# Optimization experiments

Measured on AMD Instinct MI355X. Metric: run time of the kernel, lower is better.

## Reference

```python
import jax, jax.numpy as jnp
import numpy as np

N_NODES = 20000
N_EDGES = 640000
NODE_DIM = 128
EDGE_DIM = 64
HID = 128  # must equal NODE_DIM (index_add_ into zeros_like(node_feat) in the original)
EPS = 1e-8


def setup_inputs() -> dict:
    key = jax.random.key(0)
    ks = jax.random.split(key, 16)
    s = 0.05
    return {
        "node_feat": jax.random.normal(ks[0], (N_NODES, NODE_DIM), jnp.float32),
        "edge_index": jax.random.randint(ks[1], (2, N_EDGES), 0, N_NODES, jnp.int32),
        "edge_attr": jax.random.normal(ks[2], (N_EDGES, EDGE_DIM), jnp.float32),
        "coords": jax.random.normal(ks[3], (N_NODES, 3), jnp.float32),
        # edge_mlp: Linear(2*node+edge -> hid), SiLU, Linear(hid -> hid), SiLU
        "eW1": jax.random.normal(ks[4], (2 * NODE_DIM + EDGE_DIM, HID), jnp.float32) * s,
        "eb1": jnp.zeros((HID,), jnp.float32),
        "eW2": jax.random.normal(ks[5], (HID, HID), jnp.float32) * s,
        "eb2": jnp.zeros((HID,), jnp.float32),
        # node_mlp: Linear(node+hid -> hid), SiLU, Linear(hid -> node)
        "nW1": jax.random.normal(ks[6], (NODE_DIM + HID, HID), jnp.float32) * s,
        "nb1": jnp.zeros((HID,), jnp.float32),
        "nW2": jax.random.normal(ks[7], (HID, NODE_DIM), jnp.float32) * s,
        "nb2": jnp.zeros((NODE_DIM,), jnp.float32),
        # coord_mlp: Linear(hid -> hid//2), SiLU, Linear(hid//2 -> 1)
        "cW1": jax.random.normal(ks[8], (HID, HID // 2), jnp.float32) * s,
        "cb1": jnp.zeros((HID // 2,), jnp.float32),
        "cW2": jax.random.normal(ks[9], (HID // 2, 1), jnp.float32) * s,
        "cb2": jnp.zeros((1,), jnp.float32),
    }


def reference(node_feat, edge_index, edge_attr, coords,
              eW1, eb1, eW2, eb2, nW1, nb1, nW2, nb2, cW1, cb1, cW2, cb2):
    silu = jax.nn.silu
    src, dst = edge_index[0], edge_index[1]

    # edge messages: gather -> concat -> 2-layer MLP (SiLU after both layers)
    edge_feat = jnp.concatenate([node_feat[src], node_feat[dst], edge_attr], axis=-1)  # [E, 2*node+edge]
    edge_message = silu(silu(edge_feat @ eW1 + eb1) @ eW2 + eb2)  # [E, hid]

    # aggregate messages per destination node (index_add_)
    aggr_message = jax.ops.segment_sum(edge_message, dst, num_segments=N_NODES)  # [N, hid]

    # node update (residual)
    node_input = jnp.concatenate([node_feat, aggr_message], axis=-1)
    node_update = silu(node_input @ nW1 + nb1) @ nW2 + nb2
    updated_nodes = node_feat + node_update

    # coordinate update: per-edge scalar weight times unit direction, scattered to dst
    coord_weights = silu(edge_message @ cW1 + cb1) @ cW2 + cb2  # [E, 1]
    coord_diff = coords[src] - coords[dst]  # [E, 3]
    coord_diff = coord_diff / (jnp.linalg.norm(coord_diff, axis=-1, keepdims=True) + EPS)
    coord_update = jax.ops.segment_sum(coord_weights * coord_diff, dst, num_segments=N_NODES)
    updated_coords = coords + coord_update

    return updated_nodes, updated_coords
```

## Files before the change

kernel.cpp:

```cpp
#include <hip/hip_runtime.h>
#include <math.h>

#define N_NODES 20000
#define N_EDGES 640000
#define D 128
#define ED 64
#define EPS 1e-8f
#define MT 64
#define EMT 128

#define RSTRIDE 136
#define HSTRIDE 136
#define NSTRIDE 264

#define EW2_OFF 40960
#define CW1_OFF 57344
#define NW1_OFF 65536
#define NW2_OFF 98304
#define NFBF_OFF 114688
#define CSR_OFF  2674688

typedef __attribute__((ext_vector_type(8))) short bf16x8;
typedef __attribute__((ext_vector_type(4))) short bf16x4;
typedef __attribute__((ext_vector_type(16))) float f32x16;

__device__ __forceinline__ float silu_f(float x) {
    return __fdividef(x, 1.0f + __expf(-x));
}

__device__ __forceinline__ short f2bf(float f) {
    union { float f; unsigned u; } v; v.f = f;
    unsigned r = v.u + 0x7FFFu + ((v.u >> 16) & 1u);
    return (short)(r >> 16);
}
__device__ __forceinline__ float bf2f(short s) {
    union { unsigned u; float f; } v;
    v.u = ((unsigned)(unsigned short)s) << 16;
    return v.f;
}
__device__ __forceinline__ unsigned cvt_pk_bf16(float lo, float hi) {
    unsigned r;
    asm("v_cvt_pk_bf16_f32 %0, %1, %2" : "=v"(r) : "v"(lo), "v"(hi));
    return r;
}

__global__ __launch_bounds__(256)
void prep_kernel(const float* __restrict__ eW1, const float* __restrict__ eW2,
                 const float* __restrict__ cW1, const float* __restrict__ nW1,
                 const float* __restrict__ nW2,
                 const float* __restrict__ node_feat,
                 const float* __restrict__ coords,
                 short* __restrict__ wsf, short* __restrict__ nfbf,
                 int* __restrict__ cnt,
                 float* __restrict__ nodes_io, float* __restrict__ out_coords) {
    const int t = blockIdx.x * blockDim.x + threadIdx.x;
    const int nthr = gridDim.x * blockDim.x;

    if (t < 224 * 64) {
        int f = t >> 6, lane = t & 63;
        const float* src; int kc, nt, ncol; size_t dst;
        if (f < 80)       {              src = eW1; kc = f >> 2;  nt = f & 3;  ncol = 128; dst = (size_t)f * 512; }
        else if (f < 112) { int g=f-80;  src = eW2; kc = g >> 2;  nt = g & 3;  ncol = 128; dst = EW2_OFF + (size_t)g * 512; }
        else if (f < 128) { int g=f-112; src = cW1; kc = g >> 1;  nt = g & 1;  ncol = 64;  dst = CW1_OFF + (size_t)g * 512; }
        else if (f < 192) { int g=f-128; src = nW1; kc = g >> 2;  nt = g & 3;  ncol = 128; dst = NW1_OFF + (size_t)g * 512; }
        else              { int g=f-192; src = nW2; kc = g >> 2;  nt = g & 3;  ncol = 128; dst = NW2_OFF + (size_t)g * 512; }
        int col = nt * 32 + (lane & 31);
        int k0  = kc * 16 + (lane >> 5) * 8;
        bf16x8 o;
        #pragma unroll
        for (int j = 0; j < 8; ++j) o[j] = f2bf(src[(size_t)(k0 + j) * ncol + col]);
        *(bf16x8*)&wsf[dst + (size_t)lane * 8] = o;
    }
    for (int idx = t; idx < N_NODES * D / 8; idx += nthr) {
        const float* s = node_feat + (size_t)idx * 8;
        float4 f0 = *(const float4*)s, f1 = *(const float4*)(s + 4);
        bf16x8 pk;
        pk[0]=f2bf(f0.x); pk[1]=f2bf(f0.y); pk[2]=f2bf(f0.z); pk[3]=f2bf(f0.w);
        pk[4]=f2bf(f1.x); pk[5]=f2bf(f1.y); pk[6]=f2bf(f1.z); pk[7]=f2bf(f1.w);
        *(bf16x8*)&nfbf[(size_t)idx * 8] = pk;
    }
    for (int idx = t; idx < N_NODES * D / 4; idx += nthr) {
        float4 z; z.x = 0.f; z.y = 0.f; z.z = 0.f; z.w = 0.f;
        *(float4*)&nodes_io[(size_t)idx * 4] = z;
    }
    for (int idx = t; idx < N_NODES; idx += nthr) cnt[idx] = 0;
    for (int idx = t; idx < N_NODES * 3; idx += nthr)
        out_coords[idx] = coords[idx];
}

__global__ __launch_bounds__(256)
void hist_kernel(const int* __restrict__ edge_index, int* __restrict__ cnt) {
    int t = blockIdx.x * blockDim.x + threadIdx.x;
    if (t < N_EDGES) atomicAdd(&cnt[edge_index[N_EDGES + t]], 1);
}

#define SCAN_T 1024
#define SCAN_C 20
__global__ __launch_bounds__(SCAN_T)
void scan_kernel(const int* __restrict__ cnt, int* __restrict__ cursor) {
    __shared__ int lc[N_NODES];
    __shared__ int part[SCAN_T];
    const int t = threadIdx.x;
    for (int i = t * 4; i < N_NODES; i += SCAN_T * 4)
        *(int4*)&lc[i] = *(const int4*)&cnt[i];
    __syncthreads();
    const int base = t * SCAN_C;
    int s = 0;
    #pragma unroll
    for (int i = 0; i < SCAN_C; ++i) {
        int idx = base + i;
        if (idx < N_NODES) s += lc[idx];
    }
    part[t] = s;
    __syncthreads();
    for (int off = 1; off < SCAN_T; off <<= 1) {
        int v = (t >= off) ? part[t - off] : 0;
        __syncthreads();
        part[t] += v;
        __syncthreads();
    }
    int run = part[t] - s;
    #pragma unroll
    for (int i = 0; i < SCAN_C; ++i) {
        int idx = base + i;
        if (idx < N_NODES) { int c = lc[idx]; lc[idx] = run; run += c; }
    }
    __syncthreads();
    for (int i = t * 4; i < N_NODES; i += SCAN_T * 4)
        *(int4*)&cursor[i] = *(const int4*)&lc[i];
}

__global__ __launch_bounds__(256)
void scatter_kernel(const int* __restrict__ edge_index,
                    int* __restrict__ cursor, int* __restrict__ perm) {
    int t = blockIdx.x * blockDim.x + threadIdx.x;
    if (t < N_EDGES) {
        int d = edge_index[N_EDGES + t];
        int pos = atomicAdd(&cursor[d], 1);
        perm[pos] = t;
    }
}

__global__ __launch_bounds__(256, 4)
void edge_kernel(const short* __restrict__ nfbf,
                 const int* __restrict__ edge_index,
                 const int* __restrict__ perm,
                 const float* __restrict__ edge_attr,
                 const float* __restrict__ coords,
                 const float* __restrict__ eb1, const float* __restrict__ eb2,
                 const float* __restrict__ cb1, const float* __restrict__ cW2,
                 const float* __restrict__ cb2,
                 const short* __restrict__ wsf,
                 float* __restrict__ aggr_nodes, float* __restrict__ out_coords) {
    __shared__ __align__(16) short R[EMT * RSTRIDE];
    __shared__ int s_src[EMT], s_dst[EMT];
    __shared__ float s_wgt[EMT];
    __shared__ float s_cv[EMT][3];
    __shared__ char s_segend[EMT];
    __shared__ __align__(16) float s_eb1[D], s_eb2[D];
    __shared__ __align__(16) float s_cb1[ED], s_cw2[ED];

    const int tid = threadIdx.x;
    const int E0 = blockIdx.x * EMT;

    const int ie = tid >> 1, p = tid & 1;
    const int eid  = perm[E0 + ie];
    const int esrc = edge_index[eid];
    const int edst = edge_index[N_EDGES + eid];
    if (p == 0) { s_src[ie] = esrc; s_dst[ie] = edst; }
    if (tid < EMT) s_wgt[tid] = 0.0f;
    if (tid < 128) { s_eb1[tid] = eb1[tid]; s_eb2[tid] = eb2[tid]; }
    else if (tid < 192) { int i = tid - 128; s_cb1[i] = cb1[i]; s_cw2[i] = cW2[i]; }

    {
        const short* row = nfbf + (size_t)esrc * D + p * 64;
        short* dstp = &R[ie * RSTRIDE + p * 64];
        #pragma unroll
        for (int c = 0; c < 8; ++c)
            *(bf16x8*)&dstp[c * 8] = *(const bf16x8*)&row[c * 8];
    }
    __syncthreads();
    if (tid < EMT)
        s_segend[tid] = (tid == EMT - 1) || (s_dst[tid] != s_dst[tid + 1]);

    const int lane  = tid & 63;
    const int wv    = tid >> 6;
    const int n0q   = wv & 1;
    const int m0a   = (wv >> 1) * 64;
    const int m0b   = m0a + 32;
    const int l31   = lane & 31;
    const int khalf = lane >> 5;

    const bf16x8* W1 = (const bf16x8*)wsf;
    const bf16x8* W2 = (const bf16x8*)(wsf + EW2_OFF);
    const bf16x8* W3 = (const bf16x8*)(wsf + CW1_OFF);

    f32x16 acc00, acc01, acc10, acc11;
    #pragma unroll
    for (int r = 0; r < 16; ++r) { acc00[r]=0.f; acc01[r]=0.f; acc10[r]=0.f; acc11[r]=0.f; }

    #pragma unroll
    for (int kcl = 0; kcl < 8; ++kcl) {
        bf16x8 a0 = *(const bf16x8*)&R[(m0a + l31) * RSTRIDE + kcl * 16 + khalf * 8];
        bf16x8 a1 = *(const bf16x8*)&R[(m0b + l31) * RSTRIDE + kcl * 16 + khalf * 8];
        bf16x8 b0 = W1[((kcl) * 4 + n0q * 2 + 0) * 64 + lane];
        bf16x8 b1 = W1[((kcl) * 4 + n0q * 2 + 1) * 64 + lane];
        acc00 = __builtin_amdgcn_mfma_f32_32x32x16_bf16(b0, a0, acc00, 0, 0, 0);
        acc01 = __builtin_amdgcn_mfma_f32_32x32x16_bf16(b1, a0, acc01, 0, 0, 0);
        acc10 = __builtin_amdgcn_mfma_f32_32x32x16_bf16(b0, a1, acc10, 0, 0, 0);
        acc11 = __builtin_amdgcn_mfma_f32_32x32x16_bf16(b1, a1, acc11, 0, 0, 0);
    }
    __syncthreads();

    {
        const short* row = nfbf + (size_t)edst * D + p * 64;
        short* dstp = &R[ie * RSTRIDE + p * 64];
        #pragma unroll
        for (int c = 0; c < 8; ++c)
            *(bf16x8*)&dstp[c * 8] = *(const bf16x8*)&row[c * 8];
    }
    __syncthreads();

    #pragma unroll
    for (int kcl = 0; kcl < 8; ++kcl) {
        bf16x8 a0 = *(const bf16x8*)&R[(m0a + l31) * RSTRIDE + kcl * 16 + khalf * 8];
        bf16x8 a1 = *(const bf16x8*)&R[(m0b + l31) * RSTRIDE + kcl * 16 + khalf * 8];
        bf16x8 b0 = W1[((8 + kcl) * 4 + n0q * 2 + 0) * 64 + lane];
        bf16x8 b1 = W1[((8 + kcl) * 4 + n0q * 2 + 1) * 64 + lane];
        acc00 = __builtin_amdgcn_mfma_f32_32x32x16_bf16(b0, a0, acc00, 0, 0, 0);
        acc01 = __builtin_amdgcn_mfma_f32_32x32x16_bf16(b1, a0, acc01, 0, 0, 0);
        acc10 = __builtin_amdgcn_mfma_f32_32x32x16_bf16(b0, a1, acc10, 0, 0, 0);
        acc11 = __builtin_amdgcn_mfma_f32_32x32x16_bf16(b1, a1, acc11, 0, 0, 0);
    }
    __syncthreads();

    {
        const float* arow = edge_attr + (size_t)eid * ED + p * 32;
        #pragma unroll
        for (int c = 0; c < 2; ++c) {
            float4 a0 = *(const float4*)&arow[c * 16 + 0];
            float4 a1 = *(const float4*)&arow[c * 16 + 4];
            float4 a2 = *(const float4*)&arow[c * 16 + 8];
            float4 a3 = *(const float4*)&arow[c * 16 + 12];
            uint4 q;
            q.x = cvt_pk_bf16(a0.x, a0.y); q.y = cvt_pk_bf16(a0.z, a0.w);
            q.z = cvt_pk_bf16(a1.x, a1.y); q.w = cvt_pk_bf16(a1.z, a1.w);
            *(uint4*)&R[ie * RSTRIDE + p * 32 + c * 16] = q;
            q.x = cvt_pk_bf16(a2.x, a2.y); q.y = cvt_pk_bf16(a2.z, a2.w);
            q.z = cvt_pk_bf16(a3.x, a3.y); q.w = cvt_pk_bf16(a3.z, a3.w);
            *(uint4*)&R[ie * RSTRIDE + p * 32 + c * 16 + 8] = q;
        }
    }
    __syncthreads();

    #pragma unroll
    for (int kcl = 0; kcl < 4; ++kcl) {
        bf16x8 a0 = *(const bf16x8*)&R[(m0a + l31) * RSTRIDE + kcl * 16 + khalf * 8];
        bf16x8 a1 = *(const bf16x8*)&R[(m0b + l31) * RSTRIDE + kcl * 16 + khalf * 8];
        bf16x8 b0 = W1[((16 + kcl) * 4 + n0q * 2 + 0) * 64 + lane];
        bf16x8 b1 = W1[((16 + kcl) * 4 + n0q * 2 + 1) * 64 + lane];
        acc00 = __builtin_amdgcn_mfma_f32_32x32x16_bf16(b0, a0, acc00, 0, 0, 0);
        acc01 = __builtin_amdgcn_mfma_f32_32x32x16_bf16(b1, a0, acc01, 0, 0, 0);
        acc10 = __builtin_amdgcn_mfma_f32_32x32x16_bf16(b0, a1, acc10, 0, 0, 0);
        acc11 = __builtin_amdgcn_mfma_f32_32x32x16_bf16(b1, a1, acc11, 0, 0, 0);
    }
    __syncthreads();

    #pragma unroll
    for (int mt = 0; mt < 2; ++mt) {
        int erow = (mt ? m0b : m0a) + l31;
        #pragma unroll
        for (int nt = 0; nt < 2; ++nt) {
            f32x16 A = mt ? (nt ? acc11 : acc10) : (nt ? acc01 : acc00);
            int base = n0q * 64 + nt * 32 + 4 * khalf;
            #pragma unroll
            for (int g = 0; g < 4; ++g) {
                int n = base + 8 * g;
                float4 b4 = *(const float4*)&s_eb1[n];
                uint2 dd;
                dd.x = cvt_pk_bf16(silu_f(A[4*g+0] + b4.x), silu_f(A[4*g+1] + b4.y));
                dd.y = cvt_pk_bf16(silu_f(A[4*g+2] + b4.z), silu_f(A[4*g+3] + b4.w));
                *(uint2*)&R[erow * RSTRIDE + n] = dd;
            }
        }
    }
    __syncthreads();

    #pragma unroll
    for (int r = 0; r < 16; ++r) { acc00[r]=0.f; acc01[r]=0.f; acc10[r]=0.f; acc11[r]=0.f; }
    #pragma unroll
    for (int kc = 0; kc < 8; ++kc) {
        bf16x8 a0 = *(const bf16x8*)&R[(m0a + l31) * RSTRIDE + kc * 16 + khalf * 8];
        bf16x8 a1 = *(const bf16x8*)&R[(m0b + l31) * RSTRIDE + kc * 16 + khalf * 8];
        bf16x8 b0 = W2[(kc * 4 + n0q * 2 + 0) * 64 + lane];
        bf16x8 b1 = W2[(kc * 4 + n0q * 2 + 1) * 64 + lane];
        acc00 = __builtin_amdgcn_mfma_f32_32x32x16_bf16(b0, a0, acc00, 0, 0, 0);
        acc01 = __builtin_amdgcn_mfma_f32_32x32x16_bf16(b1, a0, acc01, 0, 0, 0);
        acc10 = __builtin_amdgcn_mfma_f32_32x32x16_bf16(b0, a1, acc10, 0, 0, 0);
        acc11 = __builtin_amdgcn_mfma_f32_32x32x16_bf16(b1, a1, acc11, 0, 0, 0);
    }
    __syncthreads();

    #pragma unroll
    for (int mt = 0; mt < 2; ++mt) {
        int erow = (mt ? m0b : m0a) + l31;
        #pragma unroll
        for (int nt = 0; nt < 2; ++nt) {
            f32x16 A = mt ? (nt ? acc11 : acc10) : (nt ? acc01 : acc00);
            int base = n0q * 64 + nt * 32 + 4 * khalf;
            #pragma unroll
            for (int g = 0; g < 4; ++g) {
                int n = base + 8 * g;
                float4 b4 = *(const float4*)&s_eb2[n];
                uint2 dd;
                dd.x = cvt_pk_bf16(silu_f(A[4*g+0] + b4.x), silu_f(A[4*g+1] + b4.y));
                dd.y = cvt_pk_bf16(silu_f(A[4*g+2] + b4.z), silu_f(A[4*g+3] + b4.w));
                *(uint2*)&R[erow * RSTRIDE + n] = dd;
            }
        }
    }
    __syncthreads();

    {
        f32x16 c0, c1;
        #pragma unroll
        for (int r = 0; r < 16; ++r) { c0[r] = 0.f; c1[r] = 0.f; }
        #pragma unroll
        for (int kc = 0; kc < 8; ++kc) {
            bf16x8 a0 = *(const bf16x8*)&R[(m0a + l31) * RSTRIDE + kc * 16 + khalf * 8];
            bf16x8 a1 = *(const bf16x8*)&R[(m0b + l31) * RSTRIDE + kc * 16 + khalf * 8];
            bf16x8 b  = W3[(kc * 2 + n0q) * 64 + lane];
            c0 = __builtin_amdgcn_mfma_f32_32x32x16_bf16(b, a0, c0, 0, 0, 0);
            c1 = __builtin_amdgcn_mfma_f32_32x32x16_bf16(b, a1, c1, 0, 0, 0);
        }
        float s0 = 0.f, s1 = 0.f;
        int nb = n0q * 32 + 4 * khalf;
        #pragma unroll
        for (int g = 0; g < 4; ++g) {
            float4 b4 = *(const float4*)&s_cb1[nb + 8 * g];
            float4 w4 = *(const float4*)&s_cw2[nb + 8 * g];
            s0 += silu_f(c0[4*g+0] + b4.x) * w4.x + silu_f(c0[4*g+1] + b4.y) * w4.y
                + silu_f(c0[4*g+2] + b4.z) * w4.z + silu_f(c0[4*g+3] + b4.w) * w4.w;
            s1 += silu_f(c1[4*g+0] + b4.x) * w4.x + silu_f(c1[4*g+1] + b4.y) * w4.y
                + silu_f(c1[4*g+2] + b4.z) * w4.z + silu_f(c1[4*g+3] + b4.w) * w4.w;
        }
        s0 += __shfl_xor(s0, 32);
        s1 += __shfl_xor(s1, 32);
        if (khalf == 0) {
            atomicAdd(&s_wgt[m0a + l31], s0);
            atomicAdd(&s_wgt[m0b + l31], s1);
        }
    }
    __syncthreads();

    if (tid < EMT) {
        int e = tid;
        float wgt = s_wgt[e] + cb2[0];
        int s = s_src[e], d = s_dst[e];
        float dx = coords[s * 3 + 0] - coords[d * 3 + 0];
        float dy = coords[s * 3 + 1] - coords[d * 3 + 1];
        float dz = coords[s * 3 + 2] - coords[d * 3 + 2];
        float inv = __fdividef(wgt, sqrtf(dx * dx + dy * dy + dz * dz) + EPS);
        s_cv[e][0] = dx * inv; s_cv[e][1] = dy * inv; s_cv[e][2] = dz * inv;
    }
    __syncthreads();

    {
        int q  = tid & 31;
        int st = tid >> 5;
        int cc = q * 4;
        float a0 = 0.f, a1 = 0.f, a2 = 0.f, a3 = 0.f;
        #pragma unroll
        for (int r = 0; r < 16; ++r) {
            int e = st * 16 + r;
            bf16x4 m = *(const bf16x4*)&R[e * RSTRIDE + cc];
            a0 += bf2f(m[0]); a1 += bf2f(m[1]); a2 += bf2f(m[2]); a3 += bf2f(m[3]);
            if (s_segend[e]) {
                float* ap = &aggr_nodes[(size_t)s_dst[e] * D + cc];
                unsafeAtomicAdd(ap + 0, a0); unsafeAtomicAdd(ap + 1, a1);
                unsafeAtomicAdd(ap + 2, a2); unsafeAtomicAdd(ap + 3, a3);
                a0 = a1 = a2 = a3 = 0.f;
            }
        }
        int elast = st * 16 + 15;
        if (!s_segend[elast]) {
            float* ap = &aggr_nodes[(size_t)s_dst[elast] * D + cc];
            unsafeAtomicAdd(ap + 0, a0); unsafeAtomicAdd(ap + 1, a1);
            unsafeAtomicAdd(ap + 2, a2); unsafeAtomicAdd(ap + 3, a3);
        }
    }

    if (tid < EMT) {
        int e = tid;
        bool head = (e == 0) || (s_dst[e] != s_dst[e - 1]);
        if (head) {
            float sx = 0.f, sy = 0.f, sz = 0.f;
            int j = e;
            do {
                sx += s_cv[j][0]; sy += s_cv[j][1]; sz += s_cv[j][2];
                ++j;
            } while (j < EMT && s_dst[j] == s_dst[e]);
            int d = s_dst[e];
            unsafeAtomicAdd(&out_coords[d * 3 + 0], sx);
            unsafeAtomicAdd(&out_coords[d * 3 + 1], sy);
            unsafeAtomicAdd(&out_coords[d * 3 + 2], sz);
        }
    }
}

__global__ __launch_bounds__(256, 4)
void node_kernel(const float* __restrict__ node_feat,
                 const short* __restrict__ nfbf,
                 float* nodes_io,
                 const float* __restrict__ nb1, const float* __restrict__ nb2,
                 const short* __restrict__ wsf) {
    __shared__ __align__(16) short lds[MT * NSTRIDE];
    __shared__ __align__(16) float s_nb1[D], s_nb2[D];
    const int tid = threadIdx.x;
    const int N0 = blockIdx.x * MT;

    if (tid < 128) { s_nb1[tid] = nb1[tid]; s_nb2[tid] = nb2[tid]; }
    {
        int i = tid >> 2, p = tid & 3;
        int nid = N0 + i; if (nid > N_NODES - 1) nid = N_NODES - 1;
        const short* frow = nfbf + (size_t)nid * D;
        short* drow = &lds[i * NSTRIDE];
        #pragma unroll
        for (int c = 0; c < 4; ++c)
            *(bf16x8*)&drow[c * 32 + p * 8] = *(const bf16x8*)&frow[c * 32 + p * 8];
        const float* arow = nodes_io + (size_t)nid * D + p * 32;
        #pragma unroll
        for (int c = 0; c < 4; ++c) {
            float4 f0 = *(const float4*)&arow[c * 8];
            float4 f1 = *(const float4*)&arow[c * 8 + 4];
            bf16x8 pk;
            pk[0]=f2bf(f0.x); pk[1]=f2bf(f0.y); pk[2]=f2bf(f0.z); pk[3]=f2bf(f0.w);
            pk[4]=f2bf(f1.x); pk[5]=f2bf(f1.y); pk[6]=f2bf(f1.z); pk[7]=f2bf(f1.w);
            *(bf16x8*)&drow[128 + p * 32 + c * 8] = pk;
        }
    }
    __syncthreads();

    const int lane  = tid & 63;
    const int wv    = tid >> 6;
    const int m0    = (wv >> 1) * 32;
    const int n0q   = wv & 1;
    const int l31   = lane & 31;
    const int khalf = lane >> 5;

    const bf16x8* W1 = (const bf16x8*)(wsf + NW1_OFF);
    const bf16x8* W2 = (const bf16x8*)(wsf + NW2_OFF);

    {
        f32x16 acc0, acc1;
        #pragma unroll
        for (int r = 0; r < 16; ++r) { acc0[r] = 0.f; acc1[r] = 0.f; }
        #pragma unroll
        for (int kc = 0; kc < 16; ++kc) {
            bf16x8 a  = *(const bf16x8*)&lds[(m0 + l31) * NSTRIDE + kc * 16 + khalf * 8];
            bf16x8 b0 = W1[(kc * 4 + n0q * 2 + 0) * 64 + lane];
            bf16x8 b1 = W1[(kc * 4 + n0q * 2 + 1) * 64 + lane];
            acc0 = __builtin_amdgcn_mfma_f32_32x32x16_bf16(b0, a, acc0, 0, 0, 0);
            acc1 = __builtin_amdgcn_mfma_f32_32x32x16_bf16(b1, a, acc1, 0, 0, 0);
        }
        __syncthreads();
        int nrow = m0 + l31;
        #pragma unroll
        for (int nt = 0; nt < 2; ++nt) {
            f32x16 A = nt ? acc1 : acc0;
            int base = n0q * 64 + nt * 32 + 4 * khalf;
            #pragma unroll
            for (int g = 0; g < 4; ++g) {
                int n = base + 8 * g;
                float4 b4 = *(const float4*)&s_nb1[n];
                uint2 dd;
                dd.x = cvt_pk_bf16(silu_f(A[4*g+0] + b4.x), silu_f(A[4*g+1] + b4.y));
                dd.y = cvt_pk_bf16(silu_f(A[4*g+2] + b4.z), silu_f(A[4*g+3] + b4.w));
                *(uint2*)&lds[nrow * HSTRIDE + n] = dd;
            }
        }
    }
    __syncthreads();

    {
        f32x16 acc0, acc1;
        #pragma unroll
        for (int r = 0; r < 16; ++r) { acc0[r] = 0.f; acc1[r] = 0.f; }
        #pragma unroll
        for (int kc = 0; kc < 8; ++kc) {
            bf16x8 a  = *(const bf16x8*)&lds[(m0 + l31) * HSTRIDE + kc * 16 + khalf * 8];
            bf16x8 b0 = W2[(kc * 4 + n0q * 2 + 0) * 64 + lane];
            bf16x8 b1 = W2[(kc * 4 + n0q * 2 + 1) * 64 + lane];
            acc0 = __builtin_amdgcn_mfma_f32_32x32x16_bf16(b0, a, acc0, 0, 0, 0);
            acc1 = __builtin_amdgcn_mfma_f32_32x32x16_bf16(b1, a, acc1, 0, 0, 0);
        }
        int nid = N0 + m0 + l31;
        if (nid < N_NODES) {
            #pragma unroll
            for (int nt = 0; nt < 2; ++nt) {
                f32x16 A = nt ? acc1 : acc0;
                int base = n0q * 64 + nt * 32 + 4 * khalf;
                #pragma unroll
                for (int g = 0; g < 4; ++g) {
                    int n = base + 8 * g;
                    float4 b4  = *(const float4*)&s_nb2[n];
                    float4 rsd = *(const float4*)&node_feat[(size_t)nid * D + n];
                    float4 o;
                    o.x = A[4*g+0] + b4.x + rsd.x;
                    o.y = A[4*g+1] + b4.y + rsd.y;
                    o.z = A[4*g+2] + b4.z + rsd.z;
                    o.w = A[4*g+3] + b4.w + rsd.w;
                    *(float4*)&nodes_io[(size_t)nid * D + n] = o;
                }
            }
        }
    }
}

extern "C" void kernel_launch(void* const* d_in, const int* in_sizes, int n_in,
                              void* d_out, int out_size, void* d_ws, size_t ws_size,
                              hipStream_t stream) {
    const float* node_feat  = (const float*)d_in[0];
    const int*   edge_index = (const int*)d_in[1];
    const float* edge_attr  = (const float*)d_in[2];
    const float* coords     = (const float*)d_in[3];
    const float* eW1 = (const float*)d_in[4];
    const float* eb1 = (const float*)d_in[5];
    const float* eW2 = (const float*)d_in[6];
    const float* eb2 = (const float*)d_in[7];
    const float* nW1 = (const float*)d_in[8];
    const float* nb1 = (const float*)d_in[9];
    const float* nW2 = (const float*)d_in[10];
    const float* nb2 = (const float*)d_in[11];
    const float* cW1 = (const float*)d_in[12];
    const float* cb1 = (const float*)d_in[13];
    const float* cW2 = (const float*)d_in[14];
    const float* cb2 = (const float*)d_in[15];

    float* nodes_io   = (float*)d_out;
    float* out_coords = nodes_io + (size_t)N_NODES * D;
    short* wsf    = (short*)d_ws;
    short* nfbf   = wsf + NFBF_OFF;
    int*   cnt    = (int*)(wsf + CSR_OFF);
    int*   cursor = cnt + N_NODES;
    int*   perm   = cursor + N_NODES;

    prep_kernel<<<256, 256, 0, stream>>>(
        eW1, eW2, cW1, nW1, nW2, node_feat, coords,
        wsf, nfbf, cnt, nodes_io, out_coords);
    hist_kernel<<<N_EDGES / 256, 256, 0, stream>>>(edge_index, cnt);
    scan_kernel<<<1, SCAN_T, 0, stream>>>(cnt, cursor);
    scatter_kernel<<<N_EDGES / 256, 256, 0, stream>>>(edge_index, cursor, perm);
    edge_kernel<<<N_EDGES / EMT, 256, 0, stream>>>(
        nfbf, edge_index, perm, edge_attr, coords,
        eb1, eb2, cb1, cW2, cb2, wsf, nodes_io, out_coords);
    node_kernel<<<(N_NODES + MT - 1) / MT, 256, 0, stream>>>(
        node_feat, nfbf, nodes_io, nb1, nb2, wsf);
}
```

Measured before the change: 526.7 us.

## Give each wave full output width and chain MLP layers in registers

Result: slower. 625.0 us (+18.7%).

```diff
diff --git a/kernel.cpp b/kernel.cpp
--- a/kernel.cpp
+++ b/kernel.cpp
@@ -141,7 +141,7 @@
     }
 }
 
-__global__ __launch_bounds__(256, 4)
+__global__ __launch_bounds__(256, 3)
 void edge_kernel(const short* __restrict__ nfbf,
                  const int* __restrict__ edge_index,
                  const int* __restrict__ perm,
@@ -168,7 +168,6 @@
     const int esrc = edge_index[eid];
     const int edst = edge_index[N_EDGES + eid];
     if (p == 0) { s_src[ie] = esrc; s_dst[ie] = edst; }
-    if (tid < EMT) s_wgt[tid] = 0.0f;
     if (tid < 128) { s_eb1[tid] = eb1[tid]; s_eb2[tid] = eb2[tid]; }
     else if (tid < 192) { int i = tid - 128; s_cb1[i] = cb1[i]; s_cw2[i] = cW2[i]; }
 
@@ -185,30 +184,29 @@
 
     const int lane  = tid & 63;
     const int wv    = tid >> 6;
-    const int n0q   = wv & 1;
-    const int m0a   = (wv >> 1) * 64;
-    const int m0b   = m0a + 32;
+    const int m0    = wv * 32;
     const int l31   = lane & 31;
     const int khalf = lane >> 5;
+    const int erow  = m0 + l31;
 
     const bf16x8* W1 = (const bf16x8*)wsf;
     const bf16x8* W2 = (const bf16x8*)(wsf + EW2_OFF);
     const bf16x8* W3 = (const bf16x8*)(wsf + CW1_OFF);
 
-    f32x16 acc00, acc01, acc10, acc11;
-    #pragma unroll
-    for (int r = 0; r < 16; ++r) { acc00[r]=0.f; acc01[r]=0.f; acc10[r]=0.f; acc11[r]=0.f; }
+    f32x16 acc[4];
+    #pragma unroll
+    for (int nt = 0; nt < 4; ++nt)
+        #pragma unroll
+        for (int r = 0; r < 16; ++r) acc[nt][r] = 0.f;
 
     #pragma unroll
     for (int kcl = 0; kcl < 8; ++kcl) {
-        bf16x8 a0 = *(const bf16x8*)&R[(m0a + l31) * RSTRIDE + kcl * 16 + khalf * 8];
-        bf16x8 a1 = *(const bf16x8*)&R[(m0b + l31) * RSTRIDE + kcl * 16 + khalf * 8];
-        bf16x8 b0 = W1[((kcl) * 4 + n0q * 2 + 0) * 64 + lane];
-        bf16x8 b1 = W1[((kcl) * 4 + n0q * 2 + 1) * 64 + lane];
-        acc00 = __builtin_amdgcn_mfma_f32_32x32x16_bf16(b0, a0, acc00, 0, 0, 0);
-        acc01 = __builtin_amdgcn_mfma_f32_32x32x16_bf16(b1, a0, acc01, 0, 0, 0);
-        acc10 = __builtin_amdgcn_mfma_f32_32x32x16_bf16(b0, a1, acc10, 0, 0, 0);
-        acc11 = __builtin_amdgcn_mfma_f32_32x32x16_bf16(b1, a1, acc11, 0, 0, 0);
+        bf16x8 a = *(const bf16x8*)&R[erow * RSTRIDE + kcl * 16 + khalf * 8];
+        #pragma unroll
+        for (int nt = 0; nt < 4; ++nt) {
+            bf16x8 b = W1[(kcl * 4 + nt) * 64 + lane];
+            acc[nt] = __builtin_amdgcn_mfma_f32_32x32x16_bf16(b, a, acc[nt], 0, 0, 0);
+        }
     }
     __syncthreads();
 
@@ -223,14 +221,12 @@
 
     #pragma unroll
     for (int kcl = 0; kcl < 8; ++kcl) {
-        bf16x8 a0 = *(const bf16x8*)&R[(m0a + l31) * RSTRIDE + kcl * 16 + khalf * 8];
-        bf16x8 a1 = *(const bf16x8*)&R[(m0b + l31) * RSTRIDE + kcl * 16 + khalf * 8];
-        bf16x8 b0 = W1[((8 + kcl) * 4 + n0q * 2 + 0) * 64 + lane];
-        bf16x8 b1 = W1[((8 + kcl) * 4 + n0q * 2 + 1) * 64 + lane];
-        acc00 = __builtin_amdgcn_mfma_f32_32x32x16_bf16(b0, a0, acc00, 0, 0, 0);
-        acc01 = __builtin_amdgcn_mfma_f32_32x32x16_bf16(b1, a0, acc01, 0, 0, 0);
-        acc10 = __builtin_amdgcn_mfma_f32_32x32x16_bf16(b0, a1, acc10, 0, 0, 0);
-        acc11 = __builtin_amdgcn_mfma_f32_32x32x16_bf16(b1, a1, acc11, 0, 0, 0);
+        bf16x8 a = *(const bf16x8*)&R[erow * RSTRIDE + kcl * 16 + khalf * 8];
+        #pragma unroll
+        for (int nt = 0; nt < 4; ++nt) {
+            bf16x8 b = W1[((8 + kcl) * 4 + nt) * 64 + lane];
+            acc[nt] = __builtin_amdgcn_mfma_f32_32x32x16_bf16(b, a, acc[nt], 0, 0, 0);
+        }
     }
     __syncthreads();
 
@@ -255,101 +251,109 @@
 
     #pragma unroll
     for (int kcl = 0; kcl < 4; ++kcl) {
-        bf16x8 a0 = *(const bf16x8*)&R[(m0a + l31) * RSTRIDE + kcl * 16 + khalf * 8];
-        bf16x8 a1 = *(const bf16x8*)&R[(m0b + l31) * RSTRIDE + kcl * 16 + khalf * 8];
-        bf16x8 b0 = W1[((16 + kcl) * 4 + n0q * 2 + 0) * 64 + lane];
-        bf16x8 b1 = W1[((16 + kcl) * 4 + n0q * 2 + 1) * 64 + lane];
-        acc00 = __builtin_amdgcn_mfma_f32_32x32x16_bf16(b0, a0, acc00, 0, 0, 0);
-        acc01 = __builtin_amdgcn_mfma_f32_32x32x16_bf16(b1, a0, acc01, 0, 0, 0);
-        acc10 = __builtin_amdgcn_mfma_f32_32x32x16_bf16(b0, a1, acc10, 0, 0, 0);
-        acc11 = __builtin_amdgcn_mfma_f32_32x32x16_bf16(b1, a1, acc11, 0, 0, 0);
-    }
-    __syncthreads();
-
-    #pragma unroll
-    for (int mt = 0; mt < 2; ++mt) {
-        int erow = (mt ? m0b : m0a) + l31;
-        #pragma unroll
-        for (int nt = 0; nt < 2; ++nt) {
-            f32x16 A = mt ? (nt ? acc11 : acc10) : (nt ? acc01 : acc00);
-            int base = n0q * 64 + nt * 32 + 4 * khalf;
+        bf16x8 a = *(const bf16x8*)&R[erow * RSTRIDE + kcl * 16 + khalf * 8];
+        #pragma unroll
+        for (int nt = 0; nt < 4; ++nt) {
+            bf16x8 b = W1[((16 + kcl) * 4 + nt) * 64 + lane];
+            acc[nt] = __builtin_amdgcn_mfma_f32_32x32x16_bf16(b, a, acc[nt], 0, 0, 0);
+        }
+    }
+
+    uint2 pk[4][4];
+    #pragma unroll
+    for (int nt = 0; nt < 4; ++nt) {
+        #pragma unroll
+        for (int g = 0; g < 4; ++g) {
+            int n = nt * 32 + 4 * khalf + 8 * g;
+            float4 b4 = *(const float4*)&s_eb1[n];
+            pk[nt][g].x = cvt_pk_bf16(silu_f(acc[nt][4*g+0] + b4.x), silu_f(acc[nt][4*g+1] + b4.y));
+            pk[nt][g].y = cvt_pk_bf16(silu_f(acc[nt][4*g+2] + b4.z), silu_f(acc[nt][4*g+3] + b4.w));
+        }
+    }
+
+    {
+        f32x16 a2[4];
+        #pragma unroll
+        for (int nt = 0; nt < 4; ++nt)
+            #pragma unroll
+            for (int r = 0; r < 16; ++r) a2[nt][r] = 0.f;
+        #pragma unroll
+        for (int kc = 0; kc < 8; ++kc) {
+            const int nt = kc >> 1;
+            const int gE = (kc & 1) * 2;
+            const int gO = gE + 1;
+            uint2 own  = khalf ? pk[nt][gO] : pk[nt][gE];
+            uint2 send = khalf ? pk[nt][gE] : pk[nt][gO];
+            uint2 recv;
+            recv.x = (unsigned)__shfl_xor((int)send.x, 32);
+            recv.y = (unsigned)__shfl_xor((int)send.y, 32);
+            union { uint4 u; bf16x8 v; } fr;
+            fr.u.x = khalf ? recv.x : own.x;
+            fr.u.y = khalf ? recv.y : own.y;
+            fr.u.z = khalf ? own.x  : recv.x;
+            fr.u.w = khalf ? own.y  : recv.y;
+            #pragma unroll
+            for (int nt2 = 0; nt2 < 4; ++nt2) {
+                bf16x8 b = W2[(kc * 4 + nt2) * 64 + lane];
+                a2[nt2] = __builtin_amdgcn_mfma_f32_32x32x16_bf16(b, fr.v, a2[nt2], 0, 0, 0);
+            }
+        }
+        #pragma unroll
+        for (int nt = 0; nt < 4; ++nt) {
             #pragma unroll
             for (int g = 0; g < 4; ++g) {
-                int n = base + 8 * g;
-                float4 b4 = *(const float4*)&s_eb1[n];
-                uint2 dd;
-                dd.x = cvt_pk_bf16(silu_f(A[4*g+0] + b4.x), silu_f(A[4*g+1] + b4.y));
-                dd.y = cvt_pk_bf16(silu_f(A[4*g+2] + b4.z), silu_f(A[4*g+3] + b4.w));
-                *(uint2*)&R[erow * RSTRIDE + n] = dd;
-            }
-        }
-    }
-    __syncthreads();
-
-    #pragma unroll
-    for (int r = 0; r < 16; ++r) { acc00[r]=0.f; acc01[r]=0.f; acc10[r]=0.f; acc11[r]=0.f; }
-    #pragma unroll
-    for (int kc = 0; kc < 8; ++kc) {
-        bf16x8 a0 = *(const bf16x8*)&R[(m0a + l31) * RSTRIDE + kc * 16 + khalf * 8];
-        bf16x8 a1 = *(const bf16x8*)&R[(m0b + l31) * RSTRIDE + kc * 16 + khalf * 8];
-        bf16x8 b0 = W2[(kc * 4 + n0q * 2 + 0) * 64 + lane];
-        bf16x8 b1 = W2[(kc * 4 + n0q * 2 + 1) * 64 + lane];
-        acc00 = __builtin_amdgcn_mfma_f32_32x32x16_bf16(b0, a0, acc00, 0, 0, 0);
-        acc01 = __builtin_amdgcn_mfma_f32_32x32x16_bf16(b1, a0, acc01, 0, 0, 0);
-        acc10 = __builtin_amdgcn_mfma_f32_32x32x16_bf16(b0, a1, acc10, 0, 0, 0);
-        acc11 = __builtin_amdgcn_mfma_f32_32x32x16_bf16(b1, a1, acc11, 0, 0, 0);
-    }
-    __syncthreads();
-
-    #pragma unroll
-    for (int mt = 0; mt < 2; ++mt) {
-        int erow = (mt ? m0b : m0a) + l31;
-        #pragma unroll
-        for (int nt = 0; nt < 2; ++nt) {
-            f32x16 A = mt ? (nt ? acc11 : acc10) : (nt ? acc01 : acc00);
-            int base = n0q * 64 + nt * 32 + 4 * khalf;
+                int n = nt * 32 + 4 * khalf + 8 * g;
+                float4 b4 = *(const float4*)&s_eb2[n];
+                pk[nt][g].x = cvt_pk_bf16(silu_f(a2[nt][4*g+0] + b4.x), silu_f(a2[nt][4*g+1] + b4.y));
+                pk[nt][g].y = cvt_pk_bf16(silu_f(a2[nt][4*g+2] + b4.z), silu_f(a2[nt][4*g+3] + b4.w));
+                *(uint2*)&R[erow * RSTRIDE + n] = pk[nt][g];
+            }
+        }
+    }
+
+    {
+        f32x16 c3[2];
+        #pragma unroll
+        for (int nt3 = 0; nt3 < 2; ++nt3)
+            #pragma unroll
+            for (int r = 0; r < 16; ++r) c3[nt3][r] = 0.f;
+        #pragma unroll
+        for (int kc = 0; kc < 8; ++kc) {
+            const int nt = kc >> 1;
+            const int gE = (kc & 1) * 2;
+            const int gO = gE + 1;
+            uint2 own  = khalf ? pk[nt][gO] : pk[nt][gE];
+            uint2 send = khalf ? pk[nt][gE] : pk[nt][gO];
+            uint2 recv;
+            recv.x = (unsigned)__shfl_xor((int)send.x, 32);
+            recv.y = (unsigned)__shfl_xor((int)send.y, 32);
+            union { uint4 u; bf16x8 v; } fr;
+            fr.u.x = khalf ? recv.x : own.x;
+            fr.u.y = khalf ? recv.y : own.y;
+            fr.u.z = khalf ? own.x  : recv.x;
+            fr.u.w = khalf ? own.y  : recv.y;
+            #pragma unroll
+            for (int nt3 = 0; nt3 < 2; ++nt3) {
+                bf16x8 b = W3[(kc * 2 + nt3) * 64 + lane];
+                c3[nt3] = __builtin_amdgcn_mfma_f32_32x32x16_bf16(b, fr.v, c3[nt3], 0, 0, 0);
+            }
+        }
+        float s0 = 0.f;
+        #pragma unroll
+        for (int nt3 = 0; nt3 < 2; ++nt3) {
             #pragma unroll
             for (int g = 0; g < 4; ++g) {
-                int n = base + 8 * g;
-                float4 b4 = *(const float4*)&s_eb2[n];
-                uint2 dd;
-                dd.x = cvt_pk_bf16(silu_f(A[4*g+0] + b4.x), silu_f(A[4*g+1] + b4.y));
-                dd.y = cvt_pk_bf16(silu_f(A[4*g+2] + b4.z), silu_f(A[4*g+3] + b4.w));
-                *(uint2*)&R[erow * RSTRIDE + n] = dd;
-            }
-        }
-    }
-    __syncthreads();
-
-    {
-        f32x16 c0, c1;
-        #pragma unroll
-        for (int r = 0; r < 16; ++r) { c0[r] = 0.f; c1[r] = 0.f; }
-        #pragma unroll
-        for (int kc = 0; kc < 8; ++kc) {
-            bf16x8 a0 = *(const bf16x8*)&R[(m0a + l31) * RSTRIDE + kc * 16 + khalf * 8];
-            bf16x8 a1 = *(const bf16x8*)&R[(m0b + l31) * RSTRIDE + kc * 16 + khalf * 8];
-            bf16x8 b  = W3[(kc * 2 + n0q) * 64 + lane];
-            c0 = __builtin_amdgcn_mfma_f32_32x32x16_bf16(b, a0, c0, 0, 0, 0);
-            c1 = __builtin_amdgcn_mfma_f32_32x32x16_bf16(b, a1, c1, 0, 0, 0);
-        }
-        float s0 = 0.f, s1 = 0.f;
-        int nb = n0q * 32 + 4 * khalf;
-        #pragma unroll
-        for (int g = 0; g < 4; ++g) {
-            float4 b4 = *(const float4*)&s_cb1[nb + 8 * g];
-            float4 w4 = *(const float4*)&s_cw2[nb + 8 * g];
-            s0 += silu_f(c0[4*g+0] + b4.x) * w4.x + silu_f(c0[4*g+1] + b4.y) * w4.y
-                + silu_f(c0[4*g+2] + b4.z) * w4.z + silu_f(c0[4*g+3] + b4.w) * w4.w;
-            s1 += silu_f(c1[4*g+0] + b4.x) * w4.x + silu_f(c1[4*g+1] + b4.y) * w4.y
-                + silu_f(c1[4*g+2] + b4.z) * w4.z + silu_f(c1[4*g+3] + b4.w) * w4.w;
+                int n = nt3 * 32 + 4 * khalf + 8 * g;
+                float4 b4 = *(const float4*)&s_cb1[n];
+                float4 w4 = *(const float4*)&s_cw2[n];
+                s0 += silu_f(c3[nt3][4*g+0] + b4.x) * w4.x
+                    + silu_f(c3[nt3][4*g+1] + b4.y) * w4.y
+                    + silu_f(c3[nt3][4*g+2] + b4.z) * w4.z
+                    + silu_f(c3[nt3][4*g+3] + b4.w) * w4.w;
+            }
         }
         s0 += __shfl_xor(s0, 32);
-        s1 += __shfl_xor(s1, 32);
-        if (khalf == 0) {
-            atomicAdd(&s_wgt[m0a + l31], s0);
-            atomicAdd(&s_wgt[m0b + l31], s1);
-        }
+        if (khalf == 0) s_wgt[erow] = s0;
     }
     __syncthreads();
 
```
